# Kernel optimization log

Hardware: AMD Instinct MI355X
Metric: run time of the kernel (lower is better)

Reference implementation:

```python
import jax, jax.numpy as jnp
import numpy as np


def setup_inputs() -> dict:
    key = jax.random.key(0)
    x = jax.random.normal(key, (8, 4096, 1024), dtype=jnp.float32)
    return {"x": x}


def reference(x):
    # Causal cumulative mean over time axis: out[b,t] = mean(x[b,:t+1], axis=0)
    B, T, C = x.shape
    csum = jnp.cumsum(x, axis=1)                       # (B, T, C)
    denom = jnp.arange(1, T + 1, dtype=x.dtype)[None, :, None]
    return csum / denom
```

## Files before the change

kernel.cpp:

```cpp
#include <hip/hip_runtime.h>


constexpr int B_SZ   = 8;
constexpr int T_SZ   = 4096;
constexpr int C_SZ   = 1024;
constexpr int CHUNK  = 32;
constexpr int NCHUNK = T_SZ / CHUNK;
constexpr int C4     = C_SZ / 4;

__global__ __launch_bounds__(C4) void cummean_partial(
    const float4* __restrict__ x, float4* __restrict__ part) {
    const int k = blockIdx.x, b = blockIdx.y, c = threadIdx.x;
    const float4* xp = x + (size_t)(b * T_SZ + k * CHUNK) * C4 + c;
    float s0x=0.f,s0y=0.f,s0z=0.f,s0w=0.f, s1x=0.f,s1y=0.f,s1z=0.f,s1w=0.f;
#pragma unroll 8
    for (int t = 0; t < CHUNK; t += 2) {
        float4 a = xp[(size_t)t * C4];
        float4 d = xp[(size_t)(t + 1) * C4];
        s0x += a.x; s0y += a.y; s0z += a.z; s0w += a.w;
        s1x += d.x; s1y += d.y; s1z += d.z; s1w += d.w;
    }
    float4 s; s.x = s0x + s1x; s.y = s0y + s1y; s.z = s0z + s1z; s.w = s0w + s1w;
    part[(size_t)(b * NCHUNK + k) * C4 + c] = s;
}

__global__ __launch_bounds__(C4) void cummean_scanpart(float4* __restrict__ part) {
    const int b = blockIdx.x, c = threadIdx.x;
    float4* pp = part + (size_t)b * NCHUNK * C4 + c;
    float rx=0.f, ry=0.f, rz=0.f, rw=0.f;
#pragma unroll 4
    for (int k = 0; k < NCHUNK; ++k) {
        float4 v = pp[(size_t)k * C4];
        float4 e; e.x = rx; e.y = ry; e.z = rz; e.w = rw;
        pp[(size_t)k * C4] = e;
        rx += v.x; ry += v.y; rz += v.z; rw += v.w;
    }
}

__global__ __launch_bounds__(C4) void cummean_scan(
    const float4* __restrict__ x, const float4* __restrict__ part,
    float4* __restrict__ out) {
    const int k = blockIdx.x, b = blockIdx.y, c = threadIdx.x;

    float4 run = part[(size_t)(b * NCHUNK + k) * C4 + c];

    const size_t base = (size_t)(b * T_SZ + k * CHUNK) * C4 + c;
    const float4* xp = x + base;
    float4*       op = out + base;
    const int t0 = k * CHUNK;
#pragma unroll 8
    for (int t = 0; t < CHUNK; ++t) {
        float4 v = xp[(size_t)t * C4];
        run.x += v.x; run.y += v.y; run.z += v.z; run.w += v.w;
        const float inv = __builtin_amdgcn_rcpf((float)(t0 + t + 1));
        float4 o;
        o.x = run.x * inv; o.y = run.y * inv; o.z = run.z * inv; o.w = run.w * inv;
        op[(size_t)t * C4] = o;
    }
}

extern "C" void kernel_launch(void* const* d_in, const int* in_sizes, int n_in,
                              void* d_out, int out_size, void* d_ws, size_t ws_size,
                              hipStream_t stream) {
    const float4* x    = (const float4*)d_in[0];
    float4*       out  = (float4*)d_out;
    float4*       part = (float4*)d_ws;

    dim3 grid(NCHUNK, B_SZ);
    cummean_partial<<<grid, C4, 0, stream>>>(x, part);
    cummean_scanpart<<<B_SZ, C4, 0, stream>>>(part);
    cummean_scan<<<grid, C4, 0, stream>>>(x, part, out);
}
```

Baseline: 266.5 us.

## Drop separate partial-scan kernel; each block sums preceding chunk partials itself

Removes the middle kernel that serially scanned chunk partials with only 8 blocks. Each scan block now reads and sums all preceding chunk partials directly, a redundant prefix computation that costs up to 127 extra float4 reads per thread but cuts one launch and a poorly parallel stage. Output stores also become nontemporal so the output does not pollute the cache.

Measured after the change: 256.1 us. -3.9%, faster.

```diff
diff --git a/kernel.cpp b/kernel.cpp
--- a/kernel.cpp
+++ b/kernel.cpp
@@ -8,33 +8,22 @@
 constexpr int NCHUNK = T_SZ / CHUNK;
 constexpr int C4     = C_SZ / 4;
 
+typedef float f32x4 __attribute__((ext_vector_type(4)));
+
 __global__ __launch_bounds__(C4) void cummean_partial(
     const float4* __restrict__ x, float4* __restrict__ part) {
     const int k = blockIdx.x, b = blockIdx.y, c = threadIdx.x;
     const float4* xp = x + (size_t)(b * T_SZ + k * CHUNK) * C4 + c;
-    float s0x=0.f,s0y=0.f,s0z=0.f,s0w=0.f, s1x=0.f,s1y=0.f,s1z=0.f,s1w=0.f;
+    float sx=0.f,sy=0.f,sz=0.f,sw=0.f, tx=0.f,ty=0.f,tz=0.f,tw=0.f;
 #pragma unroll 8
     for (int t = 0; t < CHUNK; t += 2) {
         float4 a = xp[(size_t)t * C4];
         float4 d = xp[(size_t)(t + 1) * C4];
-        s0x += a.x; s0y += a.y; s0z += a.z; s0w += a.w;
-        s1x += d.x; s1y += d.y; s1z += d.z; s1w += d.w;
+        sx += a.x; sy += a.y; sz += a.z; sw += a.w;
+        tx += d.x; ty += d.y; tz += d.z; tw += d.w;
     }
-    float4 s; s.x = s0x + s1x; s.y = s0y + s1y; s.z = s0z + s1z; s.w = s0w + s1w;
+    float4 s; s.x = sx + tx; s.y = sy + ty; s.z = sz + tz; s.w = sw + tw;
     part[(size_t)(b * NCHUNK + k) * C4 + c] = s;
-}
-
-__global__ __launch_bounds__(C4) void cummean_scanpart(float4* __restrict__ part) {
-    const int b = blockIdx.x, c = threadIdx.x;
-    float4* pp = part + (size_t)b * NCHUNK * C4 + c;
-    float rx=0.f, ry=0.f, rz=0.f, rw=0.f;
-#pragma unroll 4
-    for (int k = 0; k < NCHUNK; ++k) {
-        float4 v = pp[(size_t)k * C4];
-        float4 e; e.x = rx; e.y = ry; e.z = rz; e.w = rw;
-        pp[(size_t)k * C4] = e;
-        rx += v.x; ry += v.y; rz += v.z; rw += v.w;
-    }
 }
 
 __global__ __launch_bounds__(C4) void cummean_scan(
@@ -42,20 +31,34 @@
     float4* __restrict__ out) {
     const int k = blockIdx.x, b = blockIdx.y, c = threadIdx.x;
 
-    float4 run = part[(size_t)(b * NCHUNK + k) * C4 + c];
+    float rx=0.f, ry=0.f, rz=0.f, rw=0.f, qx=0.f, qy=0.f, qz=0.f, qw=0.f;
+    const float4* pp = part + (size_t)b * NCHUNK * C4 + c;
+    int j = 0;
+    for (; j + 1 < k; j += 2) {
+        float4 a = pp[(size_t)j * C4];
+        float4 d = pp[(size_t)(j + 1) * C4];
+        rx += a.x; ry += a.y; rz += a.z; rw += a.w;
+        qx += d.x; qy += d.y; qz += d.z; qw += d.w;
+    }
+    if (j < k) {
+        float4 a = pp[(size_t)j * C4];
+        rx += a.x; ry += a.y; rz += a.z; rw += a.w;
+    }
+
+    float4 run; run.x = rx + qx; run.y = ry + qy; run.z = rz + qz; run.w = rw + qw;
 
     const size_t base = (size_t)(b * T_SZ + k * CHUNK) * C4 + c;
     const float4* xp = x + base;
-    float4*       op = out + base;
+    f32x4*        op = (f32x4*)(out + base);
     const int t0 = k * CHUNK;
 #pragma unroll 8
     for (int t = 0; t < CHUNK; ++t) {
         float4 v = xp[(size_t)t * C4];
         run.x += v.x; run.y += v.y; run.z += v.z; run.w += v.w;
         const float inv = __builtin_amdgcn_rcpf((float)(t0 + t + 1));
-        float4 o;
-        o.x = run.x * inv; o.y = run.y * inv; o.z = run.z * inv; o.w = run.w * inv;
-        op[(size_t)t * C4] = o;
+        f32x4 o;
+        o[0] = run.x * inv; o[1] = run.y * inv; o[2] = run.z * inv; o[3] = run.w * inv;
+        __builtin_nontemporal_store(o, op + (size_t)t * C4);
     }
 }
 
@@ -68,6 +71,5 @@
 
     dim3 grid(NCHUNK, B_SZ);
     cummean_partial<<<grid, C4, 0, stream>>>(x, part);
-    cummean_scanpart<<<B_SZ, C4, 0, stream>>>(part);
     cummean_scan<<<grid, C4, 0, stream>>>(x, part, out);
 }
```
